# Optimization experiments

Measured on AMD Instinct MI355X. Metric: run time of the kernel, lower is better.

## Reference

```python
import jax, jax.numpy as jnp
import numpy as np

EPS = 1e-5  # BatchNorm eps

B, LMAX = 64, 512
N_IN, N_OUT = 128, 256
LENGTHS = np.array([128 if i % 2 == 0 else 384 for i in range(B)], dtype=np.int64)  # sum = 16384
M = int(LENGTHS.sum())


def _bn(x, gamma, beta, mean, var):
    # eval-mode BatchNorm over channel (last) dim; x: [M, C]
    return (x - mean) * (gamma / jnp.sqrt(var + EPS)) + beta


def _aggregate(x, ld, am):
    # x: [M, N] ragged-concatenated node features; ld: [B] lengths; am: [B, L, L]
    # Equivalent to per-graph am[j,:l,:l] @ x_block, vectorized via zero-padding:
    # padded columns of am hit zero rows of x, and garbage rows are never gathered.
    Bn, L, _ = am.shape
    gid = jnp.repeat(jnp.arange(Bn), ld, total_repeat_length=x.shape[0])      # [M] graph id per node
    offs = jnp.concatenate([jnp.zeros((1,), ld.dtype), jnp.cumsum(ld)[:-1]])  # [B] start offsets
    pos = jnp.arange(x.shape[0]) - offs[gid]                                   # [M] within-graph position
    padded = jnp.zeros((Bn, L, x.shape[1]), x.dtype).at[gid, pos].set(x)       # [B, L, N]
    out = jnp.einsum('blm,bmn->bln', am, padded)                               # batched adjacency matmul
    return out[gid, pos]                                                       # back to ragged [M, N]


def setup_inputs() -> dict:
    key = jax.random.key(0)
    ks = jax.random.split(key, 12)
    x = jax.random.normal(ks[0], (M, N_IN, 1, 1), dtype=jnp.float32)
    ld = jnp.asarray(LENGTHS)
    am = jax.random.normal(ks[1], (B, LMAX, LMAX), dtype=jnp.float32)

    def lin_bn(kw, kb, cin, cout):
        W = jax.random.normal(kw, (cout, cin), dtype=jnp.float32) / np.sqrt(cin)
        b = jax.random.normal(kb, (cout,), dtype=jnp.float32) * 0.01
        kg, kbt, km, kv = jax.random.split(jax.random.fold_in(kw, 7), 4)
        gamma = 1.0 + 0.1 * jax.random.normal(kg, (cout,), dtype=jnp.float32)
        beta = 0.1 * jax.random.normal(kbt, (cout,), dtype=jnp.float32)
        mean = 0.1 * jax.random.normal(km, (cout,), dtype=jnp.float32)
        var = 0.5 + jax.random.uniform(kv, (cout,), dtype=jnp.float32)
        return W, b, gamma, beta, mean, var

    Wl, bl, gl, betal, ml, vl = lin_bn(ks[2], ks[3], N_IN, N_OUT)   # residual 1x1 conv + BN
    W1, b1, g1, beta1, m1, v1 = lin_bn(ks[4], ks[5], N_IN, N_IN)    # graph conv layer 1
    W2, b2, g2, beta2, m2, v2 = lin_bn(ks[6], ks[7], N_IN, N_OUT)   # graph conv layer 2
    return {
        'x': x, 'ld': ld, 'am': am,
        'Wl': Wl, 'bl': bl, 'gl': gl, 'betal': betal, 'ml': ml, 'vl': vl,
        'W1': W1, 'b1': b1, 'g1': g1, 'beta1': beta1, 'm1': m1, 'v1': v1,
        'W2': W2, 'b2': b2, 'g2': g2, 'beta2': beta2, 'm2': m2, 'v2': v2,
    }


def reference(x, ld, am,
              Wl, bl, gl, betal, ml, vl,
              W1, b1, g1, beta1, m1, v1,
              W2, b2, g2, beta2, m2, v2):
    xf = x.reshape(x.shape[0], x.shape[1])  # squeeze [M, N, 1, 1] -> [M, N]
    # residual branch (input_size != output_size): 1x1 conv + BN
    residual = _bn(xf @ Wl.T + bl, gl, betal, ml, vl)
    # graph conv layer 1: aggregate -> conv1x1 -> BN -> ReLU (dropout inactive in eval)
    h = _aggregate(xf, ld, am)
    h = jax.nn.relu(_bn(h @ W1.T + b1, g1, beta1, m1, v1))
    # graph conv layer 2: aggregate -> conv1x1 -> BN
    h = _aggregate(h, ld, am)
    h = _bn(h @ W2.T + b2, g2, beta2, m2, v2)
    out = jax.nn.leaky_relu(h + residual, negative_slope=0.01)
    return out[:, :, None, None]  # [M, N_out, 1, 1]
```

## Files before the change

kernel.cpp:

```cpp
#include <hip/hip_runtime.h>

#define EPS 1e-5f

typedef __attribute__((ext_vector_type(4))) float f32x4;
typedef __attribute__((ext_vector_type(8))) _Float16 f16x8;
typedef __attribute__((ext_vector_type(4))) _Float16 f16x4;

__device__ __forceinline__ int tidx(int r, int k, int K) {
    return (r >> 4) * (K << 4) + ((k >> 5) << 9) + ((r & 15) << 5) + (((k & 31) >> 3) << 3) + (k & 7);
}

#define MFMA16(a, b, c) __builtin_amdgcn_mfma_f32_16x16x32_f16(a, b, c, 0, 0, 0)

__device__ __forceinline__ void slot_map(int s, int& g, int& r0) {
    int c = s >> 6, j = s & 63;
    if (j < 48) { g = c * 8 + 2 * (j / 12) + 1; r0 = (j % 12) << 5; }
    else        { int jj = j - 48; g = c * 8 + 2 * (jj / 4); r0 = (jj % 4) << 5; }
}

__global__ __launch_bounds__(256) void prep_conv_kernel(
    const int* __restrict__ ld, const float* __restrict__ am,
    const float* __restrict__ Wl, const float* __restrict__ bl,
    const float* __restrict__ gl, const float* __restrict__ betal,
    const float* __restrict__ ml, const float* __restrict__ vl,
    const float* __restrict__ W1, const float* __restrict__ b1,
    const float* __restrict__ g1, const float* __restrict__ beta1,
    const float* __restrict__ m1, const float* __restrict__ v1,
    const float* __restrict__ W2, const float* __restrict__ b2,
    const float* __restrict__ g2, const float* __restrict__ beta2,
    const float* __restrict__ m2, const float* __restrict__ v2,
    int* __restrict__ offs, float* __restrict__ c1, float* __restrict__ cf,
    int* __restrict__ tg, int* __restrict__ tr, int* __restrict__ ta, int n_tasks,
    _Float16* __restrict__ W1t, _Float16* __restrict__ Wct,
    _Float16* __restrict__ amt,
    const float* __restrict__ x, _Float16* __restrict__ XTt,
    _Float16* __restrict__ xh_t, int M)
{
    __shared__ __align__(16) _Float16 Tt[128][80];
    int t = threadIdx.x;
    if (blockIdx.x < 256) {
        int m0 = blockIdx.x * 64;
        int gg = 0, off = 0;
        while (m0 >= off + ld[gg]) { off += ld[gg]; ++gg; }
        int l = ld[gg];
        #pragma unroll
        for (int p = 0; p < 8; ++p) {
            int idx = t + p * 256;
            int m = idx >> 5;
            int f = (idx & 31) * 4;
            float4 v = *(const float4*)&x[(size_t)(m0 + m) * 128 + f];
            Tt[f + 0][m] = (_Float16)v.x; Tt[f + 1][m] = (_Float16)v.y;
            Tt[f + 2][m] = (_Float16)v.z; Tt[f + 3][m] = (_Float16)v.w;
            f16x4 h;
            h[0] = (_Float16)v.x; h[1] = (_Float16)v.y;
            h[2] = (_Float16)v.z; h[3] = (_Float16)v.w;
            *(f16x4*)&xh_t[tidx(m0 + m, f, 128)] = h;
        }
        __syncthreads();
        #pragma unroll
        for (int p = 0; p < 4; ++p) {
            int idx = t + p * 256;
            int f = idx >> 3;
            int m8 = (idx & 7) * 8;
            int kl = m0 - off + m8;
            uint4 v = *(const uint4*)&Tt[f][m8];
            *(uint4*)&XTt[off * 128 + tidx(f, kl, l)] = v;
        }
    } else if (blockIdx.x < 320) {
        int b = blockIdx.x - 256;
        int gt = b * 256 + t;
        const int gsize = 64 * 256;
        if (b == 0) {
            if (t < 64) {
                int s = 0;
                for (int i = 0; i < t; ++i) s += ld[i];
                offs[t] = s;
            }
            if (t < 128) {
                float s1 = g1[t] * rsqrtf(v1[t] + EPS);
                c1[t] = (b1[t] - m1[t]) * s1 + beta1[t];
            }
            if (t < 256) {
                float s2 = g2[t] * rsqrtf(v2[t] + EPS);
                float sl = gl[t] * rsqrtf(vl[t] + EPS);
                cf[t] = (b2[t] - m2[t]) * s2 + beta2[t] + (bl[t] - ml[t]) * sl + betal[t];
            }
            for (int s = t; s < n_tasks; s += 256) {
                int g, r0;
                slot_map(s, g, r0);
                int amo = 0;
                for (int gg2 = 0; gg2 < g; ++gg2) { int L = ld[gg2]; amo += L * L; }
                tg[s] = g;
                tr[s] = r0;
                ta[s] = amo;
            }
        }
        for (int idx = gt; idx < 128 * 128; idx += gsize) {
            int n = idx >> 7, k = idx & 127;
            float s1 = g1[n] * rsqrtf(v1[n] + EPS);
            W1t[tidx(n, k, 128)] = (_Float16)(W1[idx] * s1);
        }
        for (int idx = gt; idx < 256 * 256; idx += gsize) {
            int n = idx >> 8, k = idx & 255;
            float v;
            if (k < 128) {
                float s2 = g2[n] * rsqrtf(v2[n] + EPS);
                v = W2[n * 128 + k] * s2;
            } else {
                float sl = gl[n] * rsqrtf(vl[n] + EPS);
                v = Wl[n * 128 + (k - 128)] * sl;
            }
            Wct[tidx(n, k, 256)] = (_Float16)v;
        }
    } else {
        int b2 = blockIdx.x - 320;
        int s = ((b2 & 7) << 6) + (b2 >> 3);
        int g, r0;
        slot_map(s, g, r0);
        int amo = 0;
        for (int gg2 = 0; gg2 < g; ++gg2) { int L = ld[gg2]; amo += L * L; }
        int l = ld[g];
        const float* src = am + (size_t)g * (512 * 512);
        _Float16* dst = amt + amo;
        int lq = l >> 2;
        int tot = lq << 5;
        for (int q = t; q < tot; q += 256) {
            int row = q / lq;
            int c4 = (q - row * lq) << 2;
            float4 v = *(const float4*)&src[(size_t)(r0 + row) * 512 + c4];
            f16x4 h;
            h[0] = (_Float16)v.x; h[1] = (_Float16)v.y;
            h[2] = (_Float16)v.z; h[3] = (_Float16)v.w;
            *(f16x4*)&dst[tidx(r0 + row, c4, l)] = h;
        }
    }
}

#define PHASE_A(SRC)                                                          \
    const _Float16* ap0 = SRC + off * 128 + (half * 4) * ts + lane_off + kofs;\
    const _Float16* ap1 = ap0 + ts;                                           \
    const _Float16* ap2 = ap1 + ts;                                           \
    const _Float16* ap3 = ap2 + ts;                                           \
    const _Float16* bp  = amt + ta[task] + (r0l >> 4) * ts + lane_off + kofs; \
    f32x4 acc0 = {0.f,0.f,0.f,0.f}, acc1 = acc0, acc2 = acc0, acc3 = acc0;    \
    {                                                                         \
        uint4 p0 = *(const uint4*)ap0, p1 = *(const uint4*)ap1,               \
              p2 = *(const uint4*)ap2, p3 = *(const uint4*)ap3,               \
              pb = *(const uint4*)bp;                                         \
        uint4 q0 = *(const uint4*)(ap0 + 512), q1 = *(const uint4*)(ap1 + 512),\
              q2 = *(const uint4*)(ap2 + 512), q3 = *(const uint4*)(ap3 + 512),\
              qb = *(const uint4*)(bp + 512);                                 \
        for (int s = 0; s < nkh; s += 2) {                                    \
            uint4 c0 = p0, c1v = p1, c2 = p2, c3 = p3, cb = pb;               \
            if (s + 2 < nkh) {                                                \
                int o = (s + 2) << 9;                                         \
                p0 = *(const uint4*)(ap0 + o); p1 = *(const uint4*)(ap1 + o); \
                p2 = *(const uint4*)(ap2 + o); p3 = *(const uint4*)(ap3 + o); \
                pb = *(const uint4*)(bp + o);                                 \
            }                                                                 \
            {                                                                 \
                f16x8 b = *(f16x8*)&cb;                                       \
                acc0 = MFMA16(*(f16x8*)&c0, b, acc0);                         \
                acc1 = MFMA16(*(f16x8*)&c1v, b, acc1);                        \
                acc2 = MFMA16(*(f16x8*)&c2, b, acc2);                         \
                acc3 = MFMA16(*(f16x8*)&c3, b, acc3);                         \
            }                                                                 \
            uint4 d0 = q0, d1 = q1, d2 = q2, d3 = q3, db = qb;                \
            if (s + 3 < nkh) {                                                \
                int o = (s + 3) << 9;                                         \
                q0 = *(const uint4*)(ap0 + o); q1 = *(const uint4*)(ap1 + o); \
                q2 = *(const uint4*)(ap2 + o); q3 = *(const uint4*)(ap3 + o); \
                qb = *(const uint4*)(bp + o);                                 \
            }                                                                 \
            {                                                                 \
                f16x8 b = *(f16x8*)&db;                                       \
                acc0 = MFMA16(*(f16x8*)&d0, b, acc0);                         \
                acc1 = MFMA16(*(f16x8*)&d1, b, acc1);                         \
                acc2 = MFMA16(*(f16x8*)&d2, b, acc2);                         \
                acc3 = MFMA16(*(f16x8*)&d3, b, acc3);                         \
            }                                                                 \
        }                                                                     \
    }                                                                         \
    {                                                                         \
        int fb = half * 64;                                                   \
        f32x4 aa[4] = {acc0, acc1, acc2, acc3};                               \
        _Pragma("unroll")                                                     \
        for (int i = 0; i < 4; ++i) {                                         \
            f16x4 o;                                                          \
            _Pragma("unroll")                                                 \
            for (int r = 0; r < 4; ++r) o[r] = (_Float16)aa[i][r];            \
            *(f16x4*)&Hs[kg][rt][l15][fb + i * 16 + l4 * 4] = o;              \
        }                                                                     \
    }

__global__ __launch_bounds__(512) void fused1w_kernel(
    const _Float16* __restrict__ amt, const _Float16* __restrict__ XTt,
    const int* __restrict__ ld, const int* __restrict__ offs,
    const int* __restrict__ tg, const int* __restrict__ tr, const int* __restrict__ ta,
    const _Float16* __restrict__ W1t, const float* __restrict__ bias,
    _Float16* __restrict__ H2Tt)
{
    int task = ((blockIdx.x & 7) << 6) + (blockIdx.x >> 3);
    int g = tg[task];
    int l = ld[g];
    int off = offs[g];

    int tid = threadIdx.x;
    int lane = tid & 63;
    int w = tid >> 6;
    int l15 = lane & 15;
    int l4 = lane >> 4;
    int half = w & 1;
    int rt = (w >> 1) & 1;
    int kg = w >> 2;
    int r0l = tr[task] + rt * 16;

    __shared__ __align__(16) _Float16 Hs[2][2][16][136];

    const int lane_off = (l15 << 5) + (l4 << 3);
    const int ts = l << 4;
    const int nk = l >> 5;
    const int nkh = nk >> 1;
    const int kofs = (kg * nkh) << 9;

    PHASE_A(XTt)
    __syncthreads();

    const _Float16* wbase = W1t + w * 2048 + lane_off;
    f32x4 e0 = {0.f,0.f,0.f,0.f}, e1 = e0;
    #pragma unroll
    for (int s = 0; s < 4; ++s) {
        int ho = (s << 5) + (l4 << 3);
        f16x8 b  = *(const f16x8*)(wbase + (s << 9));
        f16x8 a0 = *(const f16x8*)&Hs[0][0][l15][ho] + *(const f16x8*)&Hs[1][0][l15][ho];
        f16x8 a1 = *(const f16x8*)&Hs[0][1][l15][ho] + *(const f16x8*)&Hs[1][1][l15][ho];
        e0 = MFMA16(a0, b, e0);
        e1 = MFMA16(a1, b, e1);
    }
    int hb = off * 128;
    int trb = tr[task];
    int n = w * 16 + l15;
    float bv = bias[n];
    {
        f16x4 o;
        #pragma unroll
        for (int r = 0; r < 4; ++r) {
            float v = e0[r] + bv;
            o[r] = (_Float16)(v > 0.f ? v : 0.f);
        }
        *(f16x4*)&H2Tt[hb + tidx(n, trb + (l4 << 2), l)] = o;
    }
    {
        f16x4 o;
        #pragma unroll
        for (int r = 0; r < 4; ++r) {
            float v = e1[r] + bv;
            o[r] = (_Float16)(v > 0.f ? v : 0.f);
        }
        *(f16x4*)&H2Tt[hb + tidx(n, trb + 16 + (l4 << 2), l)] = o;
    }
}

__global__ __launch_bounds__(512) void fused2w_kernel(
    const _Float16* __restrict__ amt, const _Float16* __restrict__ H2Tt,
    const int* __restrict__ ld, const int* __restrict__ offs,
    const int* __restrict__ tg, const int* __restrict__ tr, const int* __restrict__ ta,
    const _Float16* __restrict__ xh_t, const _Float16* __restrict__ Wct,
    const float* __restrict__ bias, float* __restrict__ out)
{
    int task = ((blockIdx.x & 7) << 6) + (blockIdx.x >> 3);
    int g = tg[task];
    int l = ld[g];
    int off = offs[g];

    int tid = threadIdx.x;
    int lane = tid & 63;
    int w = tid >> 6;
    int l15 = lane & 15;
    int l4 = lane >> 4;
    int half = w & 1;
    int rt = (w >> 1) & 1;
    int kg = w >> 2;
    int r0l = tr[task] + rt * 16;

    __shared__ __align__(16) _Float16 Hs[2][2][16][136];

    const int lane_off = (l15 << 5) + (l4 << 3);
    const int ts = l << 4;
    const int nk = l >> 5;
    const int nkh = nk >> 1;
    const int kofs = (kg * nkh) << 9;

    PHASE_A(H2Tt)
    __syncthreads();

    int gmb = off + tr[task];
    const _Float16* wb0 = Wct + (w * 2) * 4096 + lane_off;
    const _Float16* wb1 = wb0 + 4096;
    const _Float16* xp0 = xh_t + (gmb >> 4) * 2048 + lane_off;
    const _Float16* xp1 = xp0 + 2048;
    f32x4 e00 = {0.f,0.f,0.f,0.f}, e01 = e00, e10 = e00, e11 = e00;
    #pragma unroll
    for (int s = 0; s < 8; ++s) {
        f16x8 a0, a1;
        if (s < 4) {
            int ho = (s << 5) + (l4 << 3);
            a0 = *(const f16x8*)&Hs[0][0][l15][ho] + *(const f16x8*)&Hs[1][0][l15][ho];
            a1 = *(const f16x8*)&Hs[0][1][l15][ho] + *(const f16x8*)&Hs[1][1][l15][ho];
        } else {
            a0 = *(const f16x8*)(xp0 + ((s - 4) << 9));
            a1 = *(const f16x8*)(xp1 + ((s - 4) << 9));
        }
        f16x8 b0 = *(const f16x8*)(wb0 + (s << 9));
        f16x8 b1 = *(const f16x8*)(wb1 + (s << 9));
        e00 = MFMA16(a0, b0, e00);
        e01 = MFMA16(a1, b0, e01);
        e10 = MFMA16(a0, b1, e10);
        e11 = MFMA16(a1, b1, e11);
    }
    int n0 = w * 32 + l15;
    int n1 = n0 + 16;
    float bv0 = bias[n0], bv1 = bias[n1];
    #pragma unroll
    for (int r = 0; r < 4; ++r) {
        int m0r = gmb + (l4 << 2) + r;
        int m1r = m0r + 16;
        float v;
        v = e00[r] + bv0; out[(size_t)m0r * 256 + n0] = v > 0.f ? v : 0.01f * v;
        v = e01[r] + bv0; out[(size_t)m1r * 256 + n0] = v > 0.f ? v : 0.01f * v;
        v = e10[r] + bv1; out[(size_t)m0r * 256 + n1] = v > 0.f ? v : 0.01f * v;
        v = e11[r] + bv1; out[(size_t)m1r * 256 + n1] = v > 0.f ? v : 0.01f * v;
    }
}

extern "C" void kernel_launch(void* const* d_in, const int* in_sizes, int n_in,
                              void* d_out, int out_size, void* d_ws, size_t ws_size,
                              hipStream_t stream) {
    const float* x     = (const float*)d_in[0];
    const int*   ld    = (const int*)d_in[1];
    const float* am    = (const float*)d_in[2];
    const float* Wl    = (const float*)d_in[3];
    const float* bl    = (const float*)d_in[4];
    const float* gl    = (const float*)d_in[5];
    const float* betal = (const float*)d_in[6];
    const float* ml    = (const float*)d_in[7];
    const float* vl    = (const float*)d_in[8];
    const float* W1    = (const float*)d_in[9];
    const float* b1    = (const float*)d_in[10];
    const float* g1    = (const float*)d_in[11];
    const float* beta1 = (const float*)d_in[12];
    const float* m1    = (const float*)d_in[13];
    const float* v1    = (const float*)d_in[14];
    const float* W2    = (const float*)d_in[15];
    const float* b2    = (const float*)d_in[16];
    const float* g2    = (const float*)d_in[17];
    const float* beta2 = (const float*)d_in[18];
    const float* m2    = (const float*)d_in[19];
    const float* v2    = (const float*)d_in[20];
    float* out = (float*)d_out;

    int M = in_sizes[0] / 128;
    int n_tasks = M / 32;

    char* w = (char*)d_ws;
    int*   offs = (int*)(w);
    float* c1   = (float*)(w + 512);
    float* cf   = (float*)(w + 1024);
    int*   tg   = (int*)(w + 2048);
    int*   tr   = (int*)(w + 4096);
    int*   ta   = (int*)(w + 6144);
    _Float16* W1t = (_Float16*)(w + 16384);
    _Float16* Wct = (_Float16*)(w + 49152);
    _Float16* amt = (_Float16*)(w + 180224);
    _Float16* XTt = (_Float16*)(w + 180224 + (size_t)10485760);
    _Float16* xh_t = XTt + (size_t)M * 128;
    _Float16* H2Tt = xh_t + (size_t)M * 128;

    prep_conv_kernel<<<832, 256, 0, stream>>>(ld, am,
        Wl, bl, gl, betal, ml, vl,
        W1, b1, g1, beta1, m1, v1,
        W2, b2, g2, beta2, m2, v2,
        offs, c1, cf, tg, tr, ta, n_tasks, W1t, Wct, amt, x, XTt, xh_t, M);

    fused1w_kernel<<<n_tasks, 512, 0, stream>>>(amt, XTt, ld, offs, tg, tr, ta, W1t, c1, H2Tt);

    fused2w_kernel<<<n_tasks, 512, 0, stream>>>(amt, H2Tt, ld, offs, tg, tr, ta, xh_t, Wct, cf, out);
}
```

Before: 43.39 us.

## Halve row tile per block to 16 and stage output through LDS for coalesced stores

Result: slower. 46.58 us (+7.4%).

```diff
diff --git a/kernel.cpp b/kernel.cpp
--- a/kernel.cpp
+++ b/kernel.cpp
@@ -12,10 +12,16 @@
 
 #define MFMA16(a, b, c) __builtin_amdgcn_mfma_f32_16x16x32_f16(a, b, c, 0, 0, 0)
 
-__device__ __forceinline__ void slot_map(int s, int& g, int& r0) {
+__device__ __forceinline__ void slot_map32(int s, int& g, int& r0) {
     int c = s >> 6, j = s & 63;
     if (j < 48) { g = c * 8 + 2 * (j / 12) + 1; r0 = (j % 12) << 5; }
     else        { int jj = j - 48; g = c * 8 + 2 * (jj / 4); r0 = (jj % 4) << 5; }
+}
+
+__device__ __forceinline__ void slot_map16(int s, int& g, int& r0) {
+    int c = s >> 7, j = s & 127;
+    if (j < 96) { g = c * 8 + 2 * (j / 24) + 1; r0 = (j % 24) << 4; }
+    else        { int jj = j - 96; g = c * 8 + 2 * (jj / 8); r0 = (jj % 8) << 4; }
 }
 
 __global__ __launch_bounds__(256) void prep_conv_kernel(
@@ -87,7 +93,7 @@
             }
             for (int s = t; s < n_tasks; s += 256) {
                 int g, r0;
-                slot_map(s, g, r0);
+                slot_map16(s, g, r0);
                 int amo = 0;
                 for (int gg2 = 0; gg2 < g; ++gg2) { int L = ld[gg2]; amo += L * L; }
                 tg[s] = g;
@@ -116,7 +122,7 @@
         int b2 = blockIdx.x - 320;
         int s = ((b2 & 7) << 6) + (b2 >> 3);
         int g, r0;
-        slot_map(s, g, r0);
+        slot_map32(s, g, r0);
         int amo = 0;
         for (int gg2 = 0; gg2 < g; ++gg2) { int L = ld[gg2]; amo += L * L; }
         int l = ld[g];
@@ -136,7 +142,7 @@
     }
 }
 
-#define PHASE_A(SRC)                                                          \
+#define PHASE_A4(SRC)                                                         \
     const _Float16* ap0 = SRC + off * 128 + (half * 4) * ts + lane_off + kofs;\
     const _Float16* ap1 = ap0 + ts;                                           \
     const _Float16* ap2 = ap1 + ts;                                           \
@@ -189,18 +195,18 @@
             f16x4 o;                                                          \
             _Pragma("unroll")                                                 \
             for (int r = 0; r < 4; ++r) o[r] = (_Float16)aa[i][r];            \
-            *(f16x4*)&Hs[kg][rt][l15][fb + i * 16 + l4 * 4] = o;              \
+            *(f16x4*)&Hs[kg][l15][fb + i * 16 + l4 * 4] = o;                  \
         }                                                                     \
     }
 
-__global__ __launch_bounds__(512) void fused1w_kernel(
+__global__ __launch_bounds__(256) void fused1w_kernel(
     const _Float16* __restrict__ amt, const _Float16* __restrict__ XTt,
     const int* __restrict__ ld, const int* __restrict__ offs,
     const int* __restrict__ tg, const int* __restrict__ tr, const int* __restrict__ ta,
     const _Float16* __restrict__ W1t, const float* __restrict__ bias,
     _Float16* __restrict__ H2Tt)
 {
-    int task = ((blockIdx.x & 7) << 6) + (blockIdx.x >> 3);
+    int task = ((blockIdx.x & 7) << 7) + (blockIdx.x >> 3);
     int g = tg[task];
     int l = ld[g];
     int off = offs[g];
@@ -211,11 +217,10 @@
     int l15 = lane & 15;
     int l4 = lane >> 4;
     int half = w & 1;
-    int rt = (w >> 1) & 1;
-    int kg = w >> 2;
-    int r0l = tr[task] + rt * 16;
-
-    __shared__ __align__(16) _Float16 Hs[2][2][16][136];
+    int kg = w >> 1;
+    int r0l = tr[task];
+
+    __shared__ __align__(16) _Float16 Hs[2][16][136];
 
     const int lane_off = (l15 << 5) + (l4 << 3);
     const int ts = l << 4;
@@ -223,52 +228,43 @@
     const int nkh = nk >> 1;
     const int kofs = (kg * nkh) << 9;
 
-    PHASE_A(XTt)
+    PHASE_A4(XTt)
     __syncthreads();
 
-    const _Float16* wbase = W1t + w * 2048 + lane_off;
+    const _Float16* wbase = W1t + (w * 2) * 2048 + lane_off;
     f32x4 e0 = {0.f,0.f,0.f,0.f}, e1 = e0;
     #pragma unroll
     for (int s = 0; s < 4; ++s) {
         int ho = (s << 5) + (l4 << 3);
-        f16x8 b  = *(const f16x8*)(wbase + (s << 9));
-        f16x8 a0 = *(const f16x8*)&Hs[0][0][l15][ho] + *(const f16x8*)&Hs[1][0][l15][ho];
-        f16x8 a1 = *(const f16x8*)&Hs[0][1][l15][ho] + *(const f16x8*)&Hs[1][1][l15][ho];
-        e0 = MFMA16(a0, b, e0);
-        e1 = MFMA16(a1, b, e1);
+        f16x8 a = *(const f16x8*)&Hs[0][l15][ho] + *(const f16x8*)&Hs[1][l15][ho];
+        e0 = MFMA16(a, *(const f16x8*)(wbase + (s << 9)),        e0);
+        e1 = MFMA16(a, *(const f16x8*)(wbase + 2048 + (s << 9)), e1);
     }
     int hb = off * 128;
-    int trb = tr[task];
-    int n = w * 16 + l15;
-    float bv = bias[n];
-    {
+    int kkb = r0l + (l4 << 2);
+    f32x4 ee[2] = {e0, e1};
+    #pragma unroll
+    for (int j = 0; j < 2; ++j) {
+        int n = w * 32 + j * 16 + l15;
+        float bv = bias[n];
         f16x4 o;
         #pragma unroll
         for (int r = 0; r < 4; ++r) {
-            float v = e0[r] + bv;
+            float v = ee[j][r] + bv;
             o[r] = (_Float16)(v > 0.f ? v : 0.f);
         }
-        *(f16x4*)&H2Tt[hb + tidx(n, trb + (l4 << 2), l)] = o;
-    }
-    {
-        f16x4 o;
-        #pragma unroll
-        for (int r = 0; r < 4; ++r) {
-            float v = e1[r] + bv;
-            o[r] = (_Float16)(v > 0.f ? v : 0.f);
-        }
-        *(f16x4*)&H2Tt[hb + tidx(n, trb + 16 + (l4 << 2), l)] = o;
-    }
-}
-
-__global__ __launch_bounds__(512) void fused2w_kernel(
+        *(f16x4*)&H2Tt[hb + tidx(n, kkb, l)] = o;
+    }
+}
+
+__global__ __launch_bounds__(256) void fused2w_kernel(
     const _Float16* __restrict__ amt, const _Float16* __restrict__ H2Tt,
     const int* __restrict__ ld, const int* __restrict__ offs,
     const int* __restrict__ tg, const int* __restrict__ tr, const int* __restrict__ ta,
     const _Float16* __restrict__ xh_t, const _Float16* __restrict__ Wct,
     const float* __restrict__ bias, float* __restrict__ out)
 {
-    int task = ((blockIdx.x & 7) << 6) + (blockIdx.x >> 3);
+    int task = ((blockIdx.x & 7) << 7) + (blockIdx.x >> 3);
     int g = tg[task];
     int l = ld[g];
     int off = offs[g];
@@ -279,11 +275,12 @@
     int l15 = lane & 15;
     int l4 = lane >> 4;
     int half = w & 1;
-    int rt = (w >> 1) & 1;
-    int kg = w >> 2;
-    int r0l = tr[task] + rt * 16;
-
-    __shared__ __align__(16) _Float16 Hs[2][2][16][136];
+    int kg = w >> 1;
+    int r0l = tr[task];
+    int gmb = off + r0l;
+
+    __shared__ __align__(16) _Float16 Hs[2][16][136];
+    __shared__ __align__(16) float OutS[16][260];
 
     const int lane_off = (l15 << 5) + (l4 << 3);
     const int ts = l << 4;
@@ -291,45 +288,46 @@
     const int nkh = nk >> 1;
     const int kofs = (kg * nkh) << 9;
 
-    PHASE_A(H2Tt)
+    PHASE_A4(H2Tt)
     __syncthreads();
 
-    int gmb = off + tr[task];
-    const _Float16* wb0 = Wct + (w * 2) * 4096 + lane_off;
-    const _Float16* wb1 = wb0 + 4096;
-    const _Float16* xp0 = xh_t + (gmb >> 4) * 2048 + lane_off;
-    const _Float16* xp1 = xp0 + 2048;
-    f32x4 e00 = {0.f,0.f,0.f,0.f}, e01 = e00, e10 = e00, e11 = e00;
+    const _Float16* wb = Wct + (w * 4) * 4096 + lane_off;
+    const _Float16* xp = xh_t + (gmb >> 4) * 2048 + lane_off;
+    f32x4 e[4];
+    #pragma unroll
+    for (int j = 0; j < 4; ++j) e[j] = (f32x4){0.f, 0.f, 0.f, 0.f};
     #pragma unroll
     for (int s = 0; s < 8; ++s) {
-        f16x8 a0, a1;
+        f16x8 a;
         if (s < 4) {
             int ho = (s << 5) + (l4 << 3);
-            a0 = *(const f16x8*)&Hs[0][0][l15][ho] + *(const f16x8*)&Hs[1][0][l15][ho];
-            a1 = *(const f16x8*)&Hs[0][1][l15][ho] + *(const f16x8*)&Hs[1][1][l15][ho];
+            a = *(const f16x8*)&Hs[0][l15][ho] + *(const f16x8*)&Hs[1][l15][ho];
         } else {
-            a0 = *(const f16x8*)(xp0 + ((s - 4) << 9));
-            a1 = *(const f16x8*)(xp1 + ((s - 4) << 9));
-        }
-        f16x8 b0 = *(const f16x8*)(wb0 + (s << 9));
-        f16x8 b1 = *(const f16x8*)(wb1 + (s << 9));
-        e00 = MFMA16(a0, b0, e00);
-        e01 = MFMA16(a1, b0, e01);
-        e10 = MFMA16(a0, b1, e10);
-        e11 = MFMA16(a1, b1, e11);
-    }
-    int n0 = w * 32 + l15;
-    int n1 = n0 + 16;
-    float bv0 = bias[n0], bv1 = bias[n1];
-    #pragma unroll
-    for (int r = 0; r < 4; ++r) {
-        int m0r = gmb + (l4 << 2) + r;
-        int m1r = m0r + 16;
-        float v;
-        v = e00[r] + bv0; out[(size_t)m0r * 256 + n0] = v > 0.f ? v : 0.01f * v;
-        v = e01[r] + bv0; out[(size_t)m1r * 256 + n0] = v > 0.f ? v : 0.01f * v;
-        v = e10[r] + bv1; out[(size_t)m0r * 256 + n1] = v > 0.f ? v : 0.01f * v;
-        v = e11[r] + bv1; out[(size_t)m1r * 256 + n1] = v > 0.f ? v : 0.01f * v;
+            a = *(const f16x8*)(xp + ((s - 4) << 9));
+        }
+        #pragma unroll
+        for (int j = 0; j < 4; ++j) {
+            f16x8 b = *(const f16x8*)(wb + j * 4096 + (s << 9));
+            e[j] = MFMA16(a, b, e[j]);
+        }
+    }
+    #pragma unroll
+    for (int j = 0; j < 4; ++j) {
+        int n = w * 64 + j * 16 + l15;
+        float bv = bias[n];
+        #pragma unroll
+        for (int r = 0; r < 4; ++r) {
+            float v = e[j][r] + bv;
+            OutS[l4 * 4 + r][n] = v > 0.f ? v : 0.01f * v;
+        }
+    }
+    __syncthreads();
+    #pragma unroll
+    for (int p = 0; p < 4; ++p) {
+        int idx = tid + p * 256;
+        int row = idx >> 6;
+        int col = (idx & 63) << 2;
+        *(float4*)&out[(size_t)(gmb + row) * 256 + col] = *(const float4*)&OutS[row][col];
     }
 }
 
@@ -360,15 +358,15 @@
     float* out = (float*)d_out;
 
     int M = in_sizes[0] / 128;
-    int n_tasks = M / 32;
+    int n_tasks = M / 16;
 
     char* w = (char*)d_ws;
     int*   offs = (int*)(w);
     float* c1   = (float*)(w + 512);
     float* cf   = (float*)(w + 1024);
     int*   tg   = (int*)(w + 2048);
-    int*   tr   = (int*)(w + 4096);
-    int*   ta   = (int*)(w + 6144);
+    int*   tr   = (int*)(w + 6144);
+    int*   ta   = (int*)(w + 10240);
     _Float16* W1t = (_Float16*)(w + 16384);
     _Float16* Wct = (_Float16*)(w + 49152);
     _Float16* amt = (_Float16*)(w + 180224);
@@ -382,7 +380,7 @@
         W2, b2, g2, beta2, m2, v2,
         offs, c1, cf, tg, tr, ta, n_tasks, W1t, Wct, amt, x, XTt, xh_t, M);
 
-    fused1w_kernel<<<n_tasks, 512, 0, stream>>>(amt, XTt, ld, offs, tg, tr, ta, W1t, c1, H2Tt);
-
-    fused2w_kernel<<<n_tasks, 512, 0, stream>>>(amt, H2Tt, ld, offs, tg, tr, ta, xh_t, Wct, cf, out);
-}
+    fused1w_kernel<<<n_tasks, 256, 0, stream>>>(amt, XTt, ld, offs, tg, tr, ta, W1t, c1, H2Tt);
+
+    fused2w_kernel<<<n_tasks, 256, 0, stream>>>(amt, H2Tt, ld, offs, tg, tr, ta, xh_t, Wct, cf, out);
+}
```

## Stage aggregation operands through double-buffered swizzled LDS instead of per-wave global loads

Applied to the files above, without the earlier changes.

Result: faster. 38.96 us (-10.2%).

```diff
diff --git a/kernel.cpp b/kernel.cpp
--- a/kernel.cpp
+++ b/kernel.cpp
@@ -136,64 +136,51 @@
     }
 }
 
-#define PHASE_A(SRC)                                                          \
-    const _Float16* ap0 = SRC + off * 128 + (half * 4) * ts + lane_off + kofs;\
-    const _Float16* ap1 = ap0 + ts;                                           \
-    const _Float16* ap2 = ap1 + ts;                                           \
-    const _Float16* ap3 = ap2 + ts;                                           \
-    const _Float16* bp  = amt + ta[task] + (r0l >> 4) * ts + lane_off + kofs; \
-    f32x4 acc0 = {0.f,0.f,0.f,0.f}, acc1 = acc0, acc2 = acc0, acc3 = acc0;    \
+#define STAGED_A()                                                            \
     {                                                                         \
-        uint4 p0 = *(const uint4*)ap0, p1 = *(const uint4*)ap1,               \
-              p2 = *(const uint4*)ap2, p3 = *(const uint4*)ap3,               \
-              pb = *(const uint4*)bp;                                         \
-        uint4 q0 = *(const uint4*)(ap0 + 512), q1 = *(const uint4*)(ap1 + 512),\
-              q2 = *(const uint4*)(ap2 + 512), q3 = *(const uint4*)(ap3 + 512),\
-              qb = *(const uint4*)(bp + 512);                                 \
-        for (int s = 0; s < nkh; s += 2) {                                    \
-            uint4 c0 = p0, c1v = p1, c2 = p2, c3 = p3, cb = pb;               \
-            if (s + 2 < nkh) {                                                \
-                int o = (s + 2) << 9;                                         \
-                p0 = *(const uint4*)(ap0 + o); p1 = *(const uint4*)(ap1 + o); \
-                p2 = *(const uint4*)(ap2 + o); p3 = *(const uint4*)(ap3 + o); \
-                pb = *(const uint4*)(bp + o);                                 \
+        uint4 cur_a = *(const uint4*)(sa);                                    \
+        uint4 cur_b; if (isB) cur_b = *(const uint4*)(sb);                    \
+        uint4 nxt_a = *(const uint4*)(sa + 512);                              \
+        uint4 nxt_b; if (isB) nxt_b = *(const uint4*)(sb + 512);              \
+        *(uint4*)&Ast[0][dstA] = cur_a;                                       \
+        if (isB) *(uint4*)&Bst[0][dstB] = cur_b;                              \
+        __syncthreads();                                                      \
+        for (int s = 0; s < nk; s += 2) {                                     \
+            uint4 fa, fb;                                                     \
+            if (s + 2 < nk) {                                                 \
+                fa = *(const uint4*)(sa + ((s + 2) << 9));                    \
+                if (isB) fb = *(const uint4*)(sb + ((s + 2) << 9));           \
             }                                                                 \
             {                                                                 \
-                f16x8 b = *(f16x8*)&cb;                                       \
-                acc0 = MFMA16(*(f16x8*)&c0, b, acc0);                         \
-                acc1 = MFMA16(*(f16x8*)&c1v, b, acc1);                        \
-                acc2 = MFMA16(*(f16x8*)&c2, b, acc2);                         \
-                acc3 = MFMA16(*(f16x8*)&c3, b, acc3);                         \
+                f16x8 a  = *(const f16x8*)&Ast[0][(w << 9) + rdo];            \
+                f16x8 b0 = *(const f16x8*)&Bst[0][rdo];                       \
+                f16x8 b1 = *(const f16x8*)&Bst[0][512 + rdo];                 \
+                acc0 = MFMA16(a, b0, acc0);                                   \
+                acc1 = MFMA16(a, b1, acc1);                                   \
             }                                                                 \
-            uint4 d0 = q0, d1 = q1, d2 = q2, d3 = q3, db = qb;                \
-            if (s + 3 < nkh) {                                                \
-                int o = (s + 3) << 9;                                         \
-                q0 = *(const uint4*)(ap0 + o); q1 = *(const uint4*)(ap1 + o); \
-                q2 = *(const uint4*)(ap2 + o); q3 = *(const uint4*)(ap3 + o); \
-                qb = *(const uint4*)(bp + o);                                 \
+            *(uint4*)&Ast[1][dstA] = nxt_a;                                   \
+            if (isB) *(uint4*)&Bst[1][dstB] = nxt_b;                          \
+            __syncthreads();                                                  \
+            if (s + 3 < nk) {                                                 \
+                nxt_a = *(const uint4*)(sa + ((s + 3) << 9));                 \
+                if (isB) nxt_b = *(const uint4*)(sb + ((s + 3) << 9));        \
             }                                                                 \
             {                                                                 \
-                f16x8 b = *(f16x8*)&db;                                       \
-                acc0 = MFMA16(*(f16x8*)&d0, b, acc0);                         \
-                acc1 = MFMA16(*(f16x8*)&d1, b, acc1);                         \
-                acc2 = MFMA16(*(f16x8*)&d2, b, acc2);                         \
-                acc3 = MFMA16(*(f16x8*)&d3, b, acc3);                         \
+                f16x8 a  = *(const f16x8*)&Ast[1][(w << 9) + rdo];            \
+                f16x8 b0 = *(const f16x8*)&Bst[1][rdo];                       \
+                f16x8 b1 = *(const f16x8*)&Bst[1][512 + rdo];                 \
+                acc0 = MFMA16(a, b0, acc0);                                   \
+                acc1 = MFMA16(a, b1, acc1);                                   \
+            }                                                                 \
+            if (s + 2 < nk) {                                                 \
+                *(uint4*)&Ast[0][dstA] = fa;                                  \
+                if (isB) *(uint4*)&Bst[0][dstB] = fb;                         \
+                __syncthreads();                                              \
             }                                                                 \
         }                                                                     \
-    }                                                                         \
-    {                                                                         \
-        int fb = half * 64;                                                   \
-        f32x4 aa[4] = {acc0, acc1, acc2, acc3};                               \
-        _Pragma("unroll")                                                     \
-        for (int i = 0; i < 4; ++i) {                                         \
-            f16x4 o;                                                          \
-            _Pragma("unroll")                                                 \
-            for (int r = 0; r < 4; ++r) o[r] = (_Float16)aa[i][r];            \
-            *(f16x4*)&Hs[kg][rt][l15][fb + i * 16 + l4 * 4] = o;              \
-        }                                                                     \
-    }
-
-__global__ __launch_bounds__(512) void fused1w_kernel(
+    }
+
+__global__ __launch_bounds__(512) void fused1s_kernel(
     const _Float16* __restrict__ amt, const _Float16* __restrict__ XTt,
     const int* __restrict__ ld, const int* __restrict__ offs,
     const int* __restrict__ tg, const int* __restrict__ tr, const int* __restrict__ ta,
@@ -210,30 +197,48 @@
     int w = tid >> 6;
     int l15 = lane & 15;
     int l4 = lane >> 4;
-    int half = w & 1;
-    int rt = (w >> 1) & 1;
-    int kg = w >> 2;
-    int r0l = tr[task] + rt * 16;
-
-    __shared__ __align__(16) _Float16 Hs[2][2][16][136];
-
-    const int lane_off = (l15 << 5) + (l4 << 3);
+
+    __shared__ __align__(16) _Float16 Ast[2][4096];
+    __shared__ __align__(16) _Float16 Bst[2][1024];
+    __shared__ __align__(16) _Float16 Hs[32][136];
+
     const int ts = l << 4;
     const int nk = l >> 5;
-    const int nkh = nk >> 1;
-    const int kofs = (kg * nkh) << 9;
-
-    PHASE_A(XTt)
+    const int lane_off = (l15 << 5) + (l4 << 3);
+    const int rdo = lane_off ^ ((l15 & 7) << 3);
+
+    int idx63 = tid & 63;
+    int wr = idx63 >> 2, wc = idx63 & 3;
+    int wt = (wr << 5) + (wc << 3);
+    int wts = wt ^ ((wr & 7) << 3);
+    const int dstA = ((tid >> 6) << 9) + wts;
+    const int dstB = (((tid >> 6) & 1) << 9) + wts;
+    const bool isB = tid < 128;
+
+    const _Float16* sa = XTt + off * 128 + (tid >> 6) * ts + (idx63 << 3);
+    const _Float16* sb = amt + ta[task]
+        + ((tr[task] >> 4) + ((tid >> 6) & 1)) * ts + (idx63 << 3);
+
+    f32x4 acc0 = {0.f, 0.f, 0.f, 0.f}, acc1 = acc0;
+    STAGED_A()
+
+    {
+        f16x4 o0, o1;
+        #pragma unroll
+        for (int r = 0; r < 4; ++r) { o0[r] = (_Float16)acc0[r]; o1[r] = (_Float16)acc1[r]; }
+        *(f16x4*)&Hs[l15][w * 16 + (l4 << 2)] = o0;
+        *(f16x4*)&Hs[16 + l15][w * 16 + (l4 << 2)] = o1;
+    }
     __syncthreads();
 
     const _Float16* wbase = W1t + w * 2048 + lane_off;
-    f32x4 e0 = {0.f,0.f,0.f,0.f}, e1 = e0;
+    f32x4 e0 = {0.f, 0.f, 0.f, 0.f}, e1 = e0;
     #pragma unroll
     for (int s = 0; s < 4; ++s) {
         int ho = (s << 5) + (l4 << 3);
+        f16x8 a0 = *(const f16x8*)&Hs[l15][ho];
+        f16x8 a1 = *(const f16x8*)&Hs[16 + l15][ho];
         f16x8 b  = *(const f16x8*)(wbase + (s << 9));
-        f16x8 a0 = *(const f16x8*)&Hs[0][0][l15][ho] + *(const f16x8*)&Hs[1][0][l15][ho];
-        f16x8 a1 = *(const f16x8*)&Hs[0][1][l15][ho] + *(const f16x8*)&Hs[1][1][l15][ho];
         e0 = MFMA16(a0, b, e0);
         e1 = MFMA16(a1, b, e1);
     }
@@ -261,7 +266,7 @@
     }
 }
 
-__global__ __launch_bounds__(512) void fused2w_kernel(
+__global__ __launch_bounds__(512) void fused2s_kernel(
     const _Float16* __restrict__ amt, const _Float16* __restrict__ H2Tt,
     const int* __restrict__ ld, const int* __restrict__ offs,
     const int* __restrict__ tg, const int* __restrict__ tr, const int* __restrict__ ta,
@@ -278,20 +283,38 @@
     int w = tid >> 6;
     int l15 = lane & 15;
     int l4 = lane >> 4;
-    int half = w & 1;
-    int rt = (w >> 1) & 1;
-    int kg = w >> 2;
-    int r0l = tr[task] + rt * 16;
-
-    __shared__ __align__(16) _Float16 Hs[2][2][16][136];
-
-    const int lane_off = (l15 << 5) + (l4 << 3);
+
+    __shared__ __align__(16) _Float16 Ast[2][4096];
+    __shared__ __align__(16) _Float16 Bst[2][1024];
+    __shared__ __align__(16) _Float16 Hs[32][136];
+
     const int ts = l << 4;
     const int nk = l >> 5;
-    const int nkh = nk >> 1;
-    const int kofs = (kg * nkh) << 9;
-
-    PHASE_A(H2Tt)
+    const int lane_off = (l15 << 5) + (l4 << 3);
+    const int rdo = lane_off ^ ((l15 & 7) << 3);
+
+    int idx63 = tid & 63;
+    int wr = idx63 >> 2, wc = idx63 & 3;
+    int wt = (wr << 5) + (wc << 3);
+    int wts = wt ^ ((wr & 7) << 3);
+    const int dstA = ((tid >> 6) << 9) + wts;
+    const int dstB = (((tid >> 6) & 1) << 9) + wts;
+    const bool isB = tid < 128;
+
+    const _Float16* sa = H2Tt + off * 128 + (tid >> 6) * ts + (idx63 << 3);
+    const _Float16* sb = amt + ta[task]
+        + ((tr[task] >> 4) + ((tid >> 6) & 1)) * ts + (idx63 << 3);
+
+    f32x4 acc0 = {0.f, 0.f, 0.f, 0.f}, acc1 = acc0;
+    STAGED_A()
+
+    {
+        f16x4 o0, o1;
+        #pragma unroll
+        for (int r = 0; r < 4; ++r) { o0[r] = (_Float16)acc0[r]; o1[r] = (_Float16)acc1[r]; }
+        *(f16x4*)&Hs[l15][w * 16 + (l4 << 2)] = o0;
+        *(f16x4*)&Hs[16 + l15][w * 16 + (l4 << 2)] = o1;
+    }
     __syncthreads();
 
     int gmb = off + tr[task];
@@ -299,14 +322,14 @@
     const _Float16* wb1 = wb0 + 4096;
     const _Float16* xp0 = xh_t + (gmb >> 4) * 2048 + lane_off;
     const _Float16* xp1 = xp0 + 2048;
-    f32x4 e00 = {0.f,0.f,0.f,0.f}, e01 = e00, e10 = e00, e11 = e00;
+    f32x4 e00 = {0.f, 0.f, 0.f, 0.f}, e01 = e00, e10 = e00, e11 = e00;
     #pragma unroll
     for (int s = 0; s < 8; ++s) {
         f16x8 a0, a1;
         if (s < 4) {
             int ho = (s << 5) + (l4 << 3);
-            a0 = *(const f16x8*)&Hs[0][0][l15][ho] + *(const f16x8*)&Hs[1][0][l15][ho];
-            a1 = *(const f16x8*)&Hs[0][1][l15][ho] + *(const f16x8*)&Hs[1][1][l15][ho];
+            a0 = *(const f16x8*)&Hs[l15][ho];
+            a1 = *(const f16x8*)&Hs[16 + l15][ho];
         } else {
             a0 = *(const f16x8*)(xp0 + ((s - 4) << 9));
             a1 = *(const f16x8*)(xp1 + ((s - 4) << 9));
@@ -382,7 +405,7 @@
         W2, b2, g2, beta2, m2, v2,
         offs, c1, cf, tg, tr, ta, n_tasks, W1t, Wct, amt, x, XTt, xh_t, M);
 
-    fused1w_kernel<<<n_tasks, 512, 0, stream>>>(amt, XTt, ld, offs, tg, tr, ta, W1t, c1, H2Tt);
-
-    fused2w_kernel<<<n_tasks, 512, 0, stream>>>(amt, H2Tt, ld, offs, tg, tr, ta, xh_t, Wct, cf, out);
-}
+    fused1s_kernel<<<n_tasks, 512, 0, stream>>>(amt, XTt, ld, offs, tg, tr, ta, W1t, c1, H2Tt);
+
+    fused2s_kernel<<<n_tasks, 512, 0, stream>>>(amt, H2Tt, ld, offs, tg, tr, ta, xh_t, Wct, cf, out);
+}
```
